# Kernel tuning notes

Hardware: AMD Instinct MI355X
Metric: run time of the kernel (lower is better)

The kernel has to match this reference:

```python
import jax, jax.numpy as jnp
import numpy as np

MANTISSA_BITS = 3  # from init_kwargs


def _bfp_quantize(x, mantissa_bits):
    """Block floating-point quantization.

    Block = the channel vector at each (n, h, w) location (axis=1 of NCHW).
    Shared exponent e is that of the block's max |value| (frexp convention:
    max_abs = m * 2^e with m in [0.5, 1)), so max_abs/2^e in [0.5, 1).
    Each element keeps `mantissa_bits` mantissa bits relative to the shared
    exponent; extra bits are truncated (toward zero), matching mantissa
    right-shift + truncation in the reference CPU/CUDA kernels.
    """
    max_abs = jnp.max(jnp.abs(x), axis=1, keepdims=True)  # [N,1,H,W]
    _, e = jnp.frexp(max_abs)                              # shared exponent per block
    delta = jnp.exp2((e - mantissa_bits).astype(x.dtype))  # quantization step
    q = jnp.trunc(x / delta) * delta
    # zero blocks quantize to zero (trunc(0)=0 already, but be explicit)
    return jnp.where(max_abs > 0, q, jnp.zeros_like(x))


def setup_inputs() -> dict:
    key = jax.random.key(0)
    activations = jax.random.normal(key, (64, 256, 56, 56), dtype=jnp.float32)
    return {"activations": activations}


def reference(activations):
    return _bfp_quantize(activations, MANTISSA_BITS)
```

## Files before the change

kernel.cpp:

```cpp
#include <hip/hip_runtime.h>
#include <cstdint>


constexpr int C    = 256;
constexpr int HW   = 56 * 56;
constexpr int HW4  = HW / 4;
constexpr int CHW4 = C * HW4;

__device__ __forceinline__ int fexp(float x) {
    int e;
    (void)frexpf(x, &e);
    return e;
}

__device__ __forceinline__ void fmax4(float4& m, const float4& v) {
    m.x = fmaxf(m.x, fabsf(v.x));
    m.y = fmaxf(m.y, fabsf(v.y));
    m.z = fmaxf(m.z, fabsf(v.z));
    m.w = fmaxf(m.w, fabsf(v.w));
}

__global__ __launch_bounds__(256, 8)
void bfp_kernel(const float4* __restrict__ in, float4* __restrict__ out) {
    const int l = threadIdx.x & 63;
    const int w = threadIdx.x >> 6;
    const int j = l & 7;
    const int g = l >> 3;

    const int s  = blockIdx.x * 8 + j;
    const int n  = s / HW4;
    const int s4 = s - n * HW4;
    const int c0 = w * 64 + g * 8;

    const float4* p = in  + (size_t)n * CHW4 + (size_t)c0 * HW4 + s4;
    float4*       q = out + (size_t)n * CHW4 + (size_t)c0 * HW4 + s4;

    float4 v0 = p[0 * HW4], v1 = p[1 * HW4], v2 = p[2 * HW4], v3 = p[3 * HW4];
    float4 v4 = p[4 * HW4], v5 = p[5 * HW4], v6 = p[6 * HW4], v7 = p[7 * HW4];

    float4 a0 = make_float4(0.f, 0.f, 0.f, 0.f), a1 = a0, a2 = a0, a3 = a0;
    fmax4(a0, v0); fmax4(a1, v1); fmax4(a2, v2); fmax4(a3, v3);
    fmax4(a0, v4); fmax4(a1, v5); fmax4(a2, v6); fmax4(a3, v7);
    float4 m;
    m.x = fmaxf(fmaxf(a0.x, a1.x), fmaxf(a2.x, a3.x));
    m.y = fmaxf(fmaxf(a0.y, a1.y), fmaxf(a2.y, a3.y));
    m.z = fmaxf(fmaxf(a0.z, a1.z), fmaxf(a2.z, a3.z));
    m.w = fmaxf(fmaxf(a0.w, a1.w), fmaxf(a2.w, a3.w));

#pragma unroll
    for (int mask = 8; mask < 64; mask <<= 1) {
        m.x = fmaxf(m.x, __shfl_xor(m.x, mask));
        m.y = fmaxf(m.y, __shfl_xor(m.y, mask));
        m.z = fmaxf(m.z, __shfl_xor(m.z, mask));
        m.w = fmaxf(m.w, __shfl_xor(m.w, mask));
    }

    __shared__ float4 red[4][8];
    if (g == 0) red[w][j] = m;
    __syncthreads();
    float4 M = red[0][j];
    fmax4(M, red[1][j]);
    fmax4(M, red[2][j]);
    fmax4(M, red[3][j]);

    const int ex = fexp(M.x), ey = fexp(M.y), ez = fexp(M.z), ew = fexp(M.w);
    const float dx = ldexpf(1.f, ex - 3), ix = ldexpf(1.f, 3 - ex);
    const float dy = ldexpf(1.f, ey - 3), iy = ldexpf(1.f, 3 - ey);
    const float dz = ldexpf(1.f, ez - 3), iz = ldexpf(1.f, 3 - ez);
    const float dw = ldexpf(1.f, ew - 3), iw = ldexpf(1.f, 3 - ew);

#define QSTORE(idx, vv)                                   \
    {                                                     \
        float4 r;                                         \
        r.x = truncf(vv.x * ix) * dx;                     \
        r.y = truncf(vv.y * iy) * dy;                     \
        r.z = truncf(vv.z * iz) * dz;                     \
        r.w = truncf(vv.w * iw) * dw;                     \
        q[idx * HW4] = r;                                 \
    }
    QSTORE(0, v0) QSTORE(1, v1) QSTORE(2, v2) QSTORE(3, v3)
    QSTORE(4, v4) QSTORE(5, v5) QSTORE(6, v6) QSTORE(7, v7)
#undef QSTORE
}

extern "C" void kernel_launch(void* const* d_in, const int* in_sizes, int n_in,
                              void* d_out, int out_size, void* d_ws, size_t ws_size,
                              hipStream_t stream) {
    const float* in = (const float*)d_in[0];
    float* out      = (float*)d_out;
    int N      = in_sizes[0] / (C * HW);
    int total4 = N * HW4;
    int blocks = total4 / 8;
    bfp_kernel<<<blocks, 256, 0, stream>>>((const float4*)in, (float4*)out);
}
```

Measured before the change: 81.59 us.

## Assign each wavefront a whole channel block and reload inputs for quantize pass

Each wavefront now owns 8 spatial float4 columns across all 256 channels (32 loads per lane), so the channel max reduces with wave shuffles only, dropping the shared-memory exchange and __syncthreads. Inputs are read twice, once for the max pass and again for quantization, instead of being held in registers. That second read is expected to mostly hit in cache, and register pressure falls. The risk is extra memory traffic if the second read misses cache, and the grid has a quarter as many blocks.

After: 305.6 us. 3.75x slower.

```diff
diff --git a/kernel.cpp b/kernel.cpp
--- a/kernel.cpp
+++ b/kernel.cpp
@@ -2,10 +2,11 @@
 #include <cstdint>
 
 
-constexpr int C    = 256;
-constexpr int HW   = 56 * 56;
-constexpr int HW4  = HW / 4;
-constexpr int CHW4 = C * HW4;
+constexpr int C      = 256;
+constexpr int HW     = 56 * 56;
+constexpr int HW4    = HW / 4;
+constexpr int CHW4   = C * HW4;
+constexpr int STRIDE = 8 * HW4;
 
 __device__ __forceinline__ int fexp(float x) {
     int e;
@@ -22,25 +23,29 @@
 
 __global__ __launch_bounds__(256, 8)
 void bfp_kernel(const float4* __restrict__ in, float4* __restrict__ out) {
-    const int l = threadIdx.x & 63;
-    const int w = threadIdx.x >> 6;
-    const int j = l & 7;
-    const int g = l >> 3;
+    const int l  = threadIdx.x & 63;
+    const int w  = threadIdx.x >> 6;
+    const int j  = l & 7;
+    const int g  = l >> 3;
+    const int sg = blockIdx.x * 4 + w;
 
-    const int s  = blockIdx.x * 8 + j;
+    const int s  = sg * 8 + j;
     const int n  = s / HW4;
     const int s4 = s - n * HW4;
-    const int c0 = w * 64 + g * 8;
 
-    const float4* p = in  + (size_t)n * CHW4 + (size_t)c0 * HW4 + s4;
-    float4*       q = out + (size_t)n * CHW4 + (size_t)c0 * HW4 + s4;
-
-    float4 v0 = p[0 * HW4], v1 = p[1 * HW4], v2 = p[2 * HW4], v3 = p[3 * HW4];
-    float4 v4 = p[4 * HW4], v5 = p[5 * HW4], v6 = p[6 * HW4], v7 = p[7 * HW4];
+    const float4* p = in  + (size_t)n * CHW4 + (size_t)g * HW4 + s4;
+    float4*       q = out + (size_t)n * CHW4 + (size_t)g * HW4 + s4;
 
     float4 a0 = make_float4(0.f, 0.f, 0.f, 0.f), a1 = a0, a2 = a0, a3 = a0;
-    fmax4(a0, v0); fmax4(a1, v1); fmax4(a2, v2); fmax4(a3, v3);
-    fmax4(a0, v4); fmax4(a1, v5); fmax4(a2, v6); fmax4(a3, v7);
+#pragma unroll
+    for (int i = 0; i < 32; i += 8) {
+        float4 x0 = p[(i + 0) * STRIDE], x1 = p[(i + 1) * STRIDE];
+        float4 x2 = p[(i + 2) * STRIDE], x3 = p[(i + 3) * STRIDE];
+        float4 x4 = p[(i + 4) * STRIDE], x5 = p[(i + 5) * STRIDE];
+        float4 x6 = p[(i + 6) * STRIDE], x7 = p[(i + 7) * STRIDE];
+        fmax4(a0, x0); fmax4(a1, x1); fmax4(a2, x2); fmax4(a3, x3);
+        fmax4(a0, x4); fmax4(a1, x5); fmax4(a2, x6); fmax4(a3, x7);
+    }
     float4 m;
     m.x = fmaxf(fmaxf(a0.x, a1.x), fmaxf(a2.x, a3.x));
     m.y = fmaxf(fmaxf(a0.y, a1.y), fmaxf(a2.y, a3.y));
@@ -55,32 +60,27 @@
         m.w = fmaxf(m.w, __shfl_xor(m.w, mask));
     }
 
-    __shared__ float4 red[4][8];
-    if (g == 0) red[w][j] = m;
-    __syncthreads();
-    float4 M = red[0][j];
-    fmax4(M, red[1][j]);
-    fmax4(M, red[2][j]);
-    fmax4(M, red[3][j]);
-
-    const int ex = fexp(M.x), ey = fexp(M.y), ez = fexp(M.z), ew = fexp(M.w);
+    const int ex = fexp(m.x), ey = fexp(m.y), ez = fexp(m.z), ew = fexp(m.w);
     const float dx = ldexpf(1.f, ex - 3), ix = ldexpf(1.f, 3 - ex);
     const float dy = ldexpf(1.f, ey - 3), iy = ldexpf(1.f, 3 - ey);
     const float dz = ldexpf(1.f, ez - 3), iz = ldexpf(1.f, 3 - ez);
     const float dw = ldexpf(1.f, ew - 3), iw = ldexpf(1.f, 3 - ew);
 
-#define QSTORE(idx, vv)                                   \
-    {                                                     \
-        float4 r;                                         \
-        r.x = truncf(vv.x * ix) * dx;                     \
-        r.y = truncf(vv.y * iy) * dy;                     \
-        r.z = truncf(vv.z * iz) * dz;                     \
-        r.w = truncf(vv.w * iw) * dw;                     \
-        q[idx * HW4] = r;                                 \
+#pragma unroll
+    for (int i = 0; i < 32; i += 8) {
+        float4 v[8];
+#pragma unroll
+        for (int k = 0; k < 8; ++k) v[k] = p[(i + k) * STRIDE];
+#pragma unroll
+        for (int k = 0; k < 8; ++k) {
+            float4 r;
+            r.x = truncf(v[k].x * ix) * dx;
+            r.y = truncf(v[k].y * iy) * dy;
+            r.z = truncf(v[k].z * iz) * dz;
+            r.w = truncf(v[k].w * iw) * dw;
+            q[(i + k) * STRIDE] = r;
+        }
     }
-    QSTORE(0, v0) QSTORE(1, v1) QSTORE(2, v2) QSTORE(3, v3)
-    QSTORE(4, v4) QSTORE(5, v5) QSTORE(6, v6) QSTORE(7, v7)
-#undef QSTORE
 }
 
 extern "C" void kernel_launch(void* const* d_in, const int* in_sizes, int n_in,
@@ -88,8 +88,7 @@
                               hipStream_t stream) {
     const float* in = (const float*)d_in[0];
     float* out      = (float*)d_out;
-    int N      = in_sizes[0] / (C * HW);
-    int total4 = N * HW4;
-    int blocks = total4 / 8;
+    int total4 = in_sizes[0] / (4 * C);
+    int blocks = total4 / 32;
     bfp_kernel<<<blocks, 256, 0, stream>>>((const float4*)in, (float4*)out);
 }
```
